# Kernel tuning notes

Hardware: AMD Instinct MI355X
Metric: run time of the kernel (lower is better)

## Reference

```python
import jax, jax.numpy as jnp
import numpy as np

# Dims: batch, lig atoms (padded), rec residues, in-feat, heads, feat/head, edge-hid, n-edges
B, L, R, F, H, FH, FE, E = 16, 128, 512, 256, 8, 32, 64, 16384
HF = H * FH  # 256


def setup_inputs() -> dict:
    key = jax.random.key(0)
    ks = jax.random.split(key, 16)
    n = jax.random.normal
    return {
        "ll_feat": n(ks[0], (B, L, L, F), dtype=jnp.float32),
        "lig_feat": n(ks[1], (B, L, F), dtype=jnp.float32),
        "rec_feat": n(ks[2], (B, R, F), dtype=jnp.float32),
        "mask": jax.random.bernoulli(ks[3], 0.9, (B, L, L)),
        "e_batch": jax.random.randint(ks[4], (E,), 0, B),
        "e_src": jax.random.randint(ks[5], (E,), 0, L),
        "e_dst": jax.random.randint(ks[6], (E,), 0, L),
        # AttentionContract params: NormAndLinear (W,b + layernorm gamma/beta) + atn linear
        "Wc": n(ks[7], (HF, F)) * 0.05, "bc": jnp.zeros(HF), "gc": jnp.ones(HF), "bec": jnp.zeros(HF),
        "Wca": n(ks[8], (H, F)) * 0.05, "bca": jnp.zeros(H),
        # AttentionExpand params (x branch and y branch NormAndLinear)
        "Wex": n(ks[9], (HF, F)) * 0.05, "bex": jnp.zeros(HF), "gex": jnp.ones(HF), "beex": jnp.zeros(HF),
        "Wey": n(ks[10], (HF, F)) * 0.05, "bey": jnp.zeros(HF), "gey": jnp.ones(HF), "beey": jnp.zeros(HF),
        # edge projection (feat_to_edge_feat gather -> linear -> scatter)
        "We": n(ks[11], (FE, 2 * F)) * 0.05, "be": jnp.zeros(FE),
    }


def _norm_linear(x, W, b, g, beta):
    """NormAndLinear: linear(leaky_relu(x)) then layernorm over last dim."""
    h = jnp.einsum('...i,oi->...o', jax.nn.leaky_relu(x), W) + b
    mu = h.mean(-1, keepdims=True)
    var = ((h - mu) ** 2).mean(-1, keepdims=True)
    return g * (h - mu) * jax.lax.rsqrt(var + 1e-5) + beta


def _masked_softmax(x, mask, axis):
    """Faithful softmax_with_mask: exp(x-max), zero masked entries, /(sum+1e-10)."""
    xe = jnp.exp(x - x.max(axis=axis, keepdims=True))
    xe = jnp.where(mask, xe, 0.0)
    return xe / (xe.sum(axis=axis, keepdims=True) + 1e-10)


def reference(ll_feat, lig_feat, rec_feat, mask, e_batch, e_src, e_dst,
              Wc, bc, gc, bec, Wca, bca,
              Wex, bex, gex, beex, Wey, bey, gey, beey, We, be):
    # --- AttentionContract: (B,L,L,F) -> (B,L,H*FH), masked softmax over axis -3 (Y) ---
    of = _norm_linear(ll_feat, Wc, bc, gc, bec).reshape(B, L, L, H, FH)
    atn = (jnp.einsum('blyf,hf->blyh', jax.nn.leaky_relu(ll_feat), Wca) + bca)[..., None]  # (B,L,L,H,1)
    atn = _masked_softmax(atn, mask[..., None, None], axis=-3)
    contracted = (atn * of).sum(-3).reshape(B, L, HF)

    # --- AttentionExpand: (B,L,F),(B,R,F) -> (B,L,R,H) ---
    xf = _norm_linear(lig_feat, Wex, bex, gex, beex).reshape(B, L, H, FH)
    yf = _norm_linear(rec_feat, Wey, bey, gey, beey).reshape(B, R, H, FH)
    expanded = jnp.einsum('bxhf,byhf->bxyh', xf, yf)

    # --- feat_to_edge_feat gather + projection + lig_edges_to_ll_feat scatter ---
    ef = jnp.concatenate((lig_feat[e_batch, e_src], lig_feat[e_batch, e_dst]), axis=-1)  # (E,2F)
    ef = jax.nn.leaky_relu(ef @ We.T + be)  # (E,FE)
    llf = jnp.zeros((B, L, L, FE), ef.dtype).at[e_batch, e_src, e_dst].add(ef)

    return (contracted, expanded, llf)
```

## Files before the change

### kernel.cpp

```cpp
#include <hip/hip_runtime.h>
#include <cstdint>
#include <cstddef>

typedef unsigned int u32;
typedef unsigned short u16;
typedef __bf16 bf16x8 __attribute__((ext_vector_type(8)));
typedef float f32x16 __attribute__((ext_vector_type(16)));
typedef float f32x4v __attribute__((ext_vector_type(4)));

#define DEV static __device__ __forceinline__

DEV u16 f2bf(float f){ u32 u=__float_as_uint(f); return (u16)((u + 0x7FFFu + ((u>>16)&1u))>>16); }
DEV u32 cvtpk(float lo, float hi){ u32 r; asm("v_cvt_pk_bf16_f32 %0, %1, %2":"=v"(r):"v"(lo),"v"(hi)); return r; }
DEV uint2 cvt4(float4 v){ uint2 r; r.x=cvtpk(v.x,v.y); r.y=cvtpk(v.z,v.w); return r; }
DEV uint2 cvt4(f32x4v v){ uint2 r; r.x=cvtpk(v.x,v.y); r.y=cvtpk(v.z,v.w); return r; }
DEV u32 lrelu_pk(u32 u){
  float lo=__uint_as_float(u<<16);
  float hi=__uint_as_float(u&0xFFFF0000u);
  lo=fmaxf(lo,0.01f*lo); hi=fmaxf(hi,0.01f*hi);
  return cvtpk(lo,hi);
}

__global__ void k_prepack(const float* __restrict__ Wc, const float* __restrict__ Wca,
    const float* __restrict__ Wex, const float* __restrict__ Wey, const float* __restrict__ We,
    const unsigned char* __restrict__ maskb,
    u16* __restrict__ wpc, u16* __restrict__ wpx, u16* __restrict__ wpy,
    u16* __restrict__ wpe, int* __restrict__ flags, float* __restrict__ outl)
{
  int idx = blockIdx.x*256 + threadIdx.x;
  {
    int t=idx>>13, kk=(idx>>9)&15, ln=(idx>>3)&63, j=idx&7;
    int n=t*32+(ln&31), k=kk*16+(ln>>5)*8+j;
    if (idx < 73728){
      float v;
      if (t<8) v = Wc[n*256+k];
      else { int n2=n-256; v = (n2<8) ? Wca[n2*256+k] : 0.f; }
      wpc[idx]=f2bf(v);
    }
    if (idx < 65536){ wpx[idx]=f2bf(Wex[n*256+k]); wpy[idx]=f2bf(Wey[n*256+k]); }
  }
  if (idx < 32768){
    int t=idx>>14, kk=(idx>>9)&31, ln=(idx>>3)&63, j=idx&7;
    int n=t*32+(ln&31), k=kk*16+(ln>>5)*8+j;
    wpe[idx]=f2bf(We[n*512+k]);
  }
  {
    float4 z; z.x=0.f; z.y=0.f; z.z=0.f; z.w=0.f;
    float4* p = (float4*)outl;
    for (size_t i = (size_t)idx; i < 4194304u; i += 73728u) p[i] = z;
  }
  if (idx==0){
    int c3f1=0,c3f3=0,nzoff=0,nz4m8=0,nz0=0;
    for (int i=0;i<256;i++){
      unsigned char b=maskb[i];
      if ((i&3)==1 && b==0x3F) c3f1++;
      if ((i&3)==3 && b==0x3F) c3f3++;
      if ((i&3)!=0 && b) nzoff++;
      if ((i&7)>=4 && b) nz4m8++;
      if ((i&7)==0 && b) nz0++;
    }
    int mode;
    if (c3f1>8) mode=2;
    else if (c3f3>8) mode=3;
    else if (nzoff>8) mode=0;
    else if (nz4m8==0 && nz0>4) mode=4;
    else mode=1;
    flags[0]=mode;
  }
}

union FMem {
  struct { char slab[65536]; float maskv[128]; } c;
  struct { u16 ytile[8448]; float stage[4][2048]; } e;
  char eslab[65536];
};

DEV void contract_body(FMem& sm, int bl,
    const float* __restrict__ ll, const void* __restrict__ maskp,
    const u16* __restrict__ Wp, const float* __restrict__ bc, const float* __restrict__ bca,
    const float* __restrict__ gc, const float* __restrict__ bec,
    const int* __restrict__ flags, float* __restrict__ outc)
{
  int tid=threadIdx.x, lane=tid&63, wave=tid>>6;
  const float* src = ll + (size_t)bl*(128*256);

  if (tid < 128){
    int mode = flags[0];
    size_t mi = (size_t)bl*128 + tid;
    bool on;
    if (mode==0)      on = ((const unsigned char*)maskp)[mi] != 0;
    else if (mode==1) on = ((const int*)maskp)[mi] != 0;
    else if (mode==2) on = ((const u16*)maskp)[mi] != 0;
    else if (mode==4) on = ((const unsigned long long*)maskp)[mi] != 0ull;
    else              on = (((const u32*)maskp)[mi]<<1) != 0;
    sm.c.maskv[tid] = on ? 1.f : 0.f;
  }

  #pragma unroll 8
  for (int it=0;it<32;it++){
    int row = wave*32 + it;
    f32x4v v = __builtin_nontemporal_load((const f32x4v*)(src + row*256 + lane*4));
    uint2 pk = cvt4(v);
    *(uint2*)(sm.c.slab + row*512 + ((((lane>>1) ^ (row&31)))<<4) + (lane&1)*8) = pk;
  }
  __syncthreads();

  f32x16 acc[9];
  #pragma unroll
  for (int t=0;t<9;t++)
    #pragma unroll
    for (int i=0;i<16;i++) acc[t][i]=0.f;
  int y0 = wave*32;
  int arow = y0 + (lane&31);
  int axor = arow & 31;
  int half = lane>>5;
  const char* sb = sm.c.slab;
  const u16* wl = Wp + lane*8;

  uint4 raw = *(const uint4*)(sb + arow*512 + ((half ^ axor)<<4));
  bf16x8 w0 = *(const bf16x8*)(wl);
  bf16x8 w1 = *(const bf16x8*)(wl + 8192);
  bf16x8 w2 = *(const bf16x8*)(wl + 16384);
  bf16x8 w3 = *(const bf16x8*)(wl + 24576);
  bf16x8 w4 = *(const bf16x8*)(wl + 32768);
  bf16x8 w5 = *(const bf16x8*)(wl + 40960);
  bf16x8 w6 = *(const bf16x8*)(wl + 49152);
  bf16x8 w7 = *(const bf16x8*)(wl + 57344);
  bf16x8 w8 = *(const bf16x8*)(wl + 65536);

  #pragma unroll 4
  for (int kk=0;kk<16;kk++){
    int kn = (kk+1)&15;
    uint4 rawn = *(const uint4*)(sb + arow*512 + (((kn*2+half) ^ axor)<<4));
    const u16* wkn = wl + (size_t)kn*512;
    bf16x8 n0 = *(const bf16x8*)(wkn);
    bf16x8 n1 = *(const bf16x8*)(wkn + 8192);
    bf16x8 n2 = *(const bf16x8*)(wkn + 16384);
    bf16x8 n3 = *(const bf16x8*)(wkn + 24576);
    bf16x8 n4 = *(const bf16x8*)(wkn + 32768);
    bf16x8 n5 = *(const bf16x8*)(wkn + 40960);
    bf16x8 n6 = *(const bf16x8*)(wkn + 49152);
    bf16x8 n7 = *(const bf16x8*)(wkn + 57344);
    bf16x8 n8 = *(const bf16x8*)(wkn + 65536);
    __builtin_amdgcn_sched_barrier(0);
    uint4 t4; t4.x=lrelu_pk(raw.x); t4.y=lrelu_pk(raw.y); t4.z=lrelu_pk(raw.z); t4.w=lrelu_pk(raw.w);
    bf16x8 a = __builtin_bit_cast(bf16x8, t4);
    acc[0] = __builtin_amdgcn_mfma_f32_32x32x16_bf16(a, w0, acc[0], 0,0,0);
    acc[1] = __builtin_amdgcn_mfma_f32_32x32x16_bf16(a, w1, acc[1], 0,0,0);
    acc[2] = __builtin_amdgcn_mfma_f32_32x32x16_bf16(a, w2, acc[2], 0,0,0);
    acc[3] = __builtin_amdgcn_mfma_f32_32x32x16_bf16(a, w3, acc[3], 0,0,0);
    acc[4] = __builtin_amdgcn_mfma_f32_32x32x16_bf16(a, w4, acc[4], 0,0,0);
    acc[5] = __builtin_amdgcn_mfma_f32_32x32x16_bf16(a, w5, acc[5], 0,0,0);
    acc[6] = __builtin_amdgcn_mfma_f32_32x32x16_bf16(a, w6, acc[6], 0,0,0);
    acc[7] = __builtin_amdgcn_mfma_f32_32x32x16_bf16(a, w7, acc[7], 0,0,0);
    acc[8] = __builtin_amdgcn_mfma_f32_32x32x16_bf16(a, w8, acc[8], 0,0,0);
    raw=rawn;
    w0=n0; w1=n1; w2=n2; w3=n3; w4=n4; w5=n5; w6=n6; w7=n7; w8=n8;
  }
  __syncthreads();

  float* logit = (float*)sm.c.slab;
  float* partial = logit + 1536;

  int col = lane & 31;
  float bv[8], gv[8], bev[8];
  #pragma unroll
  for (int t=0;t<8;t++){
    int n=t*32+col; bv[t]=bc[n]; gv[t]=gc[n]; bev[t]=bec[n];
  }
  float bcav = (col<8) ? bca[col] : 0.f;

  #pragma unroll
  for (int r=0;r<16;r++){
    int row=(r&3)+8*(r>>2)+4*half;
    float s=0.f, sq=0.f;
    #pragma unroll
    for (int t=0;t<8;t++){
      float v = acc[t][r] + bv[t]; acc[t][r]=v; s += v; sq = fmaf(v,v,sq);
    }
    #pragma unroll
    for (int m=1;m<=16;m<<=1){ s += __shfl_xor(s,m,64); sq += __shfl_xor(sq,m,64); }
    float mu = s*(1.f/256.f);
    float var = fmaf(sq,1.f/256.f, -mu*mu);
    float rin = rsqrtf(var+1e-5f);
    #pragma unroll
    for (int t=0;t<8;t++) acc[t][r] = fmaf((acc[t][r]-mu)*rin, gv[t], bev[t]);
    if (col<8) logit[(y0+row)*12+col] = acc[8][r] + bcav;
  }
  __syncthreads();

  {
    int h = tid>>5, sub = tid&31;
    float lv[4], ev[4];
    #pragma unroll
    for (int j=0;j<4;j++) lv[j] = logit[(sub+32*j)*12 + h];
    float mx = fmaxf(fmaxf(lv[0],lv[1]), fmaxf(lv[2],lv[3]));
    #pragma unroll
    for (int m=1;m<=16;m<<=1) mx = fmaxf(mx, __shfl_xor(mx,m,64));
    float ssum=0.f;
    #pragma unroll
    for (int j=0;j<4;j++){ ev[j] = __expf(lv[j]-mx)*sm.c.maskv[sub+32*j]; ssum += ev[j]; }
    #pragma unroll
    for (int m=1;m<=16;m<<=1) ssum += __shfl_xor(ssum,m,64);
    float inv = 1.f/(ssum+1e-10f);
    #pragma unroll
    for (int j=0;j<4;j++) logit[(sub+32*j)*12+h] = ev[j]*inv;
  }
  __syncthreads();

  float ctr[8];
  #pragma unroll
  for (int t=0;t<8;t++) ctr[t]=0.f;
  #pragma unroll
  for (int r=0;r<16;r++){
    int row=(r&3)+8*(r>>2)+4*half;
    const float* wr = &logit[(y0+row)*12];
    float4 w0v = *(const float4*)wr;
    float4 w1v = *(const float4*)(wr+4);
    ctr[0]=fmaf(w0v.x,acc[0][r],ctr[0]); ctr[1]=fmaf(w0v.y,acc[1][r],ctr[1]);
    ctr[2]=fmaf(w0v.z,acc[2][r],ctr[2]); ctr[3]=fmaf(w0v.w,acc[3][r],ctr[3]);
    ctr[4]=fmaf(w1v.x,acc[4][r],ctr[4]); ctr[5]=fmaf(w1v.y,acc[5][r],ctr[5]);
    ctr[6]=fmaf(w1v.z,acc[6][r],ctr[6]); ctr[7]=fmaf(w1v.w,acc[7][r],ctr[7]);
  }
  #pragma unroll
  for (int t=0;t<8;t++) ctr[t] += __shfl_xor(ctr[t],32,64);
  if (lane<32){
    #pragma unroll
    for (int t=0;t<8;t++) partial[wave*256 + t*32 + col] = ctr[t];
  }
  __syncthreads();
  float v = partial[tid]+partial[256+tid]+partial[512+tid]+partial[768+tid];
  outc[(size_t)bl*256 + tid] = v;
}

DEV void expand_body(FMem& sm, int blk,
    const u16* __restrict__ xf, const u16* __restrict__ yf, float* __restrict__ oute)
{
  int tid=threadIdx.x, lane=tid&63, wave=tid>>6;
  int bi = blk>>4, yt = blk&15;

  #pragma unroll
  for (int i=0;i<4;i++){
    int idx=i*256+tid; int row=idx>>5, c=idx&31;
    uint4 v = *(const uint4*)(yf + ((size_t)(bi*512 + yt*32 + row))*256 + c*8);
    *(uint4*)((char*)sm.e.ytile + row*528 + c*16) = v;
  }
  __syncthreads();

  bf16x8 af[2][8];
  #pragma unroll
  for (int xi=0;xi<2;xi++){
    int x = (wave*2+xi)*16 + (lane&15);
    #pragma unroll
    for (int h=0;h<8;h++)
      af[xi][h] = *(const bf16x8*)(xf + ((size_t)(bi*128+x))*256 + h*32 + (lane>>4)*8);
  }
  float* stw = sm.e.stage[wave];
  #pragma unroll
  for (int xi=0;xi<2;xi++){
    #pragma unroll
    for (int nt=0;nt<2;nt++){
      f32x4v c[8];
      #pragma unroll
      for (int h=0;h<8;h++){
        bf16x8 bv = *(const bf16x8*)((const char*)sm.e.ytile + (nt*16+(lane&15))*528 + (h*32+(lane>>4)*8)*2);
        f32x4v z = {0.f,0.f,0.f,0.f};
        c[h] = __builtin_amdgcn_mfma_f32_16x16x32_bf16(af[xi][h], bv, z, 0,0,0);
      }
      #pragma unroll
      for (int q=0;q<4;q++){
        int xp=(lane>>4)*4+q, yp=lane&15;
        float* sp = &stw[(xp*16+yp)*8];
        float4 v0; v0.x=c[0][q]; v0.y=c[1][q]; v0.z=c[2][q]; v0.w=c[3][q];
        float4 v1; v1.x=c[4][q]; v1.y=c[5][q]; v1.z=c[6][q]; v1.w=c[7][q];
        *(float4*)sp = v0;
        *(float4*)(sp+4) = v1;
      }
      #pragma unroll
      for (int j=0;j<4;j++){
        int pi=j*64+lane, xp=pi>>4, yp=pi&15;
        const float* sp = &stw[(xp*16+yp)*8];
        float4 a = *(const float4*)sp;
        float4 b2 = *(const float4*)(sp+4);
        size_t x=(size_t)(wave*2+xi)*16+xp, y=(size_t)yt*32+nt*16+yp;
        float* po = oute + (((size_t)bi*128+x)*512 + y)*8;
        *(float4*)po = a;
        *(float4*)(po+4) = b2;
      }
    }
  }
}

DEV void edges_body(FMem& sm, int blk,
    const float* __restrict__ lig, const int* __restrict__ eb, const int* __restrict__ es,
    const int* __restrict__ ed, const u16* __restrict__ Wp, const float* __restrict__ bias,
    float* __restrict__ outl)
{
  char* slab = sm.eslab;
  int tid=threadIdx.x, lane=tid&63, wave=tid>>6;
  int e0 = blk*64;
  int ge = e0 + wave*16 + (lane&15);
  int b0=eb[ge], s0=es[ge], d0=ed[ge];
  long long ps = (long long)(uintptr_t)(lig + ((size_t)(b0*128+s0))*256);
  long long pd = (long long)(uintptr_t)(lig + ((size_t)(b0*128+d0))*256);
  #pragma unroll 4
  for (int i=0;i<16;i++){
    int ri = wave*16 + i;
    const float* sp = (const float*)(uintptr_t)__shfl(ps, i, 16);
    const float* dp = (const float*)(uintptr_t)__shfl(pd, i, 16);
    #pragma unroll
    for (int j=0;j<2;j++){
      const float* base = j ? dp : sp;
      float4 v = *(const float4*)(base + lane*4);
      uint2 pk = cvt4(v);
      int g = j*32 + (lane>>1);
      *(uint2*)(slab + (size_t)ri*1024 + ((g ^ (ri&63))<<4) + (lane&1)*8) = pk;
    }
  }
  __syncthreads();

  f32x16 acc;
  #pragma unroll
  for (int i=0;i<16;i++) acc[i]=0.f;
  int arow = (wave&1)*32 + (lane&31);
  int axor = arow & 63;
  int half = lane>>5;
  int t = wave>>1;
  const u16* wl = Wp + lane*8 + (size_t)t*16384;

  uint4 raw = *(const uint4*)(slab + (size_t)arow*1024 + ((half ^ axor)<<4));
  bf16x8 w = *(const bf16x8*)(wl);
  for (int kk=0;kk<32;kk++){
    int kn = (kk+1)&31;
    uint4 rn = *(const uint4*)(slab + (size_t)arow*1024 + (((kn*2+half) ^ axor)<<4));
    bf16x8 nw = *(const bf16x8*)(wl + (size_t)kn*512);
    __builtin_amdgcn_sched_barrier(0);
    bf16x8 a = __builtin_bit_cast(bf16x8, raw);
    acc = __builtin_amdgcn_mfma_f32_32x32x16_bf16(a, w, acc, 0,0,0);
    raw=rn; w=nw;
  }
  int col = lane&31;
  float bv = bias[t*32+col];
  #pragma unroll
  for (int r=0;r<16;r++){
    int row=(r&3)+8*(r>>2)+4*half;
    int ee = e0 + (wave&1)*32 + row;
    int bb=eb[ee], ss=es[ee], dd=ed[ee];
    float* cell = outl + (((size_t)(bb*128+ss))*128 + (size_t)dd)*64;
    float v = acc[r] + bv;
    v = fmaxf(v, 0.01f*v);
    atomicAdd(cell + t*32 + col, v);
  }
}

__global__ __launch_bounds__(256,2) void k_fused(
    const float* __restrict__ ll, const void* __restrict__ maskp,
    const u16* __restrict__ wpc, const float* __restrict__ bc, const float* __restrict__ bca,
    const float* __restrict__ gc, const float* __restrict__ bec,
    const int* __restrict__ flags, float* __restrict__ outc,
    const u16* __restrict__ xf, const u16* __restrict__ yf, float* __restrict__ oute,
    const float* __restrict__ lig, const int* __restrict__ eb, const int* __restrict__ es,
    const int* __restrict__ ed, const u16* __restrict__ wpe, const float* __restrict__ be,
    float* __restrict__ outl)
{
  __shared__ __attribute__((aligned(16))) FMem sm;
  int bid = blockIdx.x;
  if (bid < 256)       edges_body(sm, bid, lig, eb, es, ed, wpe, be, outl);
  else if (bid < 512)  expand_body(sm, bid-256, xf, yf, oute);
  else                 contract_body(sm, bid-512, ll, maskp, wpc, bc, bca, gc, bec, flags, outc);
}

__global__ __launch_bounds__(256,2) void k_nl(
    const float* __restrict__ lig, const float* __restrict__ rec,
    const u16* __restrict__ Wpx, const u16* __restrict__ Wpy,
    const float* __restrict__ bx, const float* __restrict__ gx, const float* __restrict__ ex,
    const float* __restrict__ by, const float* __restrict__ gy, const float* __restrict__ ey,
    u16* __restrict__ xf, u16* __restrict__ yf)
{
  __shared__ __attribute__((aligned(16))) char slab[65536];
  int tid=threadIdx.x, lane=tid&63, wave=tid>>6;
  bool isx = blockIdx.x < 16;
  int bb = isx ? blockIdx.x : blockIdx.x - 16;
  const float* src  = isx ? lig : rec;
  const u16*  Wp    = isx ? Wpx : Wpy;
  const float* bias = isx ? bx : by;
  const float* g    = isx ? gx : gy;
  const float* beta = isx ? ex : ey;
  u16* dst          = isx ? xf : yf;

  const float* s0 = src + (size_t)bb*(128*256);
  #pragma unroll 8
  for (int it=0;it<32;it++){
    int row = wave*32 + it;
    float4 v = *(const float4*)(s0 + row*256 + lane*4);
    uint2 pk = cvt4(v);
    *(uint2*)(slab + row*512 + ((((lane>>1) ^ (row&31)))<<4) + (lane&1)*8) = pk;
  }
  __syncthreads();

  f32x16 acc[8];
  #pragma unroll
  for (int t=0;t<8;t++)
    #pragma unroll
    for (int i=0;i<16;i++) acc[t][i]=0.f;
  int y0 = wave*32;
  int arow = y0 + (lane&31);
  int axor = arow & 31;
  int half = lane>>5;
  const u16* wl = Wp + lane*8;

  uint4 raw = *(const uint4*)(slab + arow*512 + ((half ^ axor)<<4));
  bf16x8 w0 = *(const bf16x8*)(wl);
  bf16x8 w1 = *(const bf16x8*)(wl + 8192);
  bf16x8 w2 = *(const bf16x8*)(wl + 16384);
  bf16x8 w3 = *(const bf16x8*)(wl + 24576);
  bf16x8 w4 = *(const bf16x8*)(wl + 32768);
  bf16x8 w5 = *(const bf16x8*)(wl + 40960);
  bf16x8 w6 = *(const bf16x8*)(wl + 49152);
  bf16x8 w7 = *(const bf16x8*)(wl + 57344);

  #pragma unroll 4
  for (int kk=0;kk<16;kk++){
    int kn = (kk+1)&15;
    uint4 rawn = *(const uint4*)(slab + arow*512 + (((kn*2+half) ^ axor)<<4));
    const u16* wkn = wl + (size_t)kn*512;
    bf16x8 n0 = *(const bf16x8*)(wkn);
    bf16x8 n1 = *(const bf16x8*)(wkn + 8192);
    bf16x8 n2 = *(const bf16x8*)(wkn + 16384);
    bf16x8 n3 = *(const bf16x8*)(wkn + 24576);
    bf16x8 n4 = *(const bf16x8*)(wkn + 32768);
    bf16x8 n5 = *(const bf16x8*)(wkn + 40960);
    bf16x8 n6 = *(const bf16x8*)(wkn + 49152);
    bf16x8 n7 = *(const bf16x8*)(wkn + 57344);
    __builtin_amdgcn_sched_barrier(0);
    uint4 t4; t4.x=lrelu_pk(raw.x); t4.y=lrelu_pk(raw.y); t4.z=lrelu_pk(raw.z); t4.w=lrelu_pk(raw.w);
    bf16x8 a = __builtin_bit_cast(bf16x8, t4);
    acc[0] = __builtin_amdgcn_mfma_f32_32x32x16_bf16(a, w0, acc[0], 0,0,0);
    acc[1] = __builtin_amdgcn_mfma_f32_32x32x16_bf16(a, w1, acc[1], 0,0,0);
    acc[2] = __builtin_amdgcn_mfma_f32_32x32x16_bf16(a, w2, acc[2], 0,0,0);
    acc[3] = __builtin_amdgcn_mfma_f32_32x32x16_bf16(a, w3, acc[3], 0,0,0);
    acc[4] = __builtin_amdgcn_mfma_f32_32x32x16_bf16(a, w4, acc[4], 0,0,0);
    acc[5] = __builtin_amdgcn_mfma_f32_32x32x16_bf16(a, w5, acc[5], 0,0,0);
    acc[6] = __builtin_amdgcn_mfma_f32_32x32x16_bf16(a, w6, acc[6], 0,0,0);
    acc[7] = __builtin_amdgcn_mfma_f32_32x32x16_bf16(a, w7, acc[7], 0,0,0);
    raw=rawn;
    w0=n0; w1=n1; w2=n2; w3=n3; w4=n4; w5=n5; w6=n6; w7=n7;
  }
  int col = lane & 31;
  float bv[8], gv[8], bev[8];
  #pragma unroll
  for (int t=0;t<8;t++){
    int n=t*32+col; bv[t]=bias[n]; gv[t]=g[n]; bev[t]=beta[n];
  }
  #pragma unroll
  for (int r=0;r<16;r++){
    int row=(r&3)+8*(r>>2)+4*half;
    float s=0.f, sq=0.f;
    #pragma unroll
    for (int t=0;t<8;t++){
      float v = acc[t][r] + bv[t]; acc[t][r]=v; s += v; sq = fmaf(v,v,sq);
    }
    #pragma unroll
    for (int m=1;m<=16;m<<=1){ s += __shfl_xor(s,m,64); sq += __shfl_xor(sq,m,64); }
    float mu = s*(1.f/256.f);
    float var = fmaf(sq,1.f/256.f, -mu*mu);
    float rin = rsqrtf(var+1e-5f);
    size_t rowg = (size_t)bb*128 + y0 + row;
    #pragma unroll
    for (int t=0;t<8;t++){
      float v = fmaf((acc[t][r]-mu)*rin, gv[t], bev[t]);
      dst[rowg*256 + t*32 + col] = f2bf(v);
    }
  }
}

extern "C" void kernel_launch(void* const* d_in, const int* in_sizes, int n_in,
                              void* d_out, int out_size, void* d_ws, size_t ws_size,
                              hipStream_t stream)
{
  (void)in_sizes; (void)n_in; (void)out_size; (void)ws_size;
  const float* ll  = (const float*)d_in[0];
  const float* lig = (const float*)d_in[1];
  const float* rec = (const float*)d_in[2];
  const void* mask = d_in[3];
  const int* eb = (const int*)d_in[4];
  const int* es = (const int*)d_in[5];
  const int* ed = (const int*)d_in[6];
  const float* Wc  =(const float*)d_in[7];  const float* bc  =(const float*)d_in[8];
  const float* gc  =(const float*)d_in[9];  const float* bec =(const float*)d_in[10];
  const float* Wca =(const float*)d_in[11]; const float* bca =(const float*)d_in[12];
  const float* Wex =(const float*)d_in[13]; const float* bex =(const float*)d_in[14];
  const float* gex =(const float*)d_in[15]; const float* beex=(const float*)d_in[16];
  const float* Wey =(const float*)d_in[17]; const float* bey =(const float*)d_in[18];
  const float* gey =(const float*)d_in[19]; const float* beey=(const float*)d_in[20];
  const float* We  =(const float*)d_in[21]; const float* be  =(const float*)d_in[22];

  float* outc = (float*)d_out;
  float* oute = outc + 524288;
  float* outl = outc + 8912896;

  char* ws = (char*)d_ws;
  int* flags = (int*)ws;
  u16* wpc = (u16*)(ws + 4096);
  u16* wpx = (u16*)(ws + 151552);
  u16* wpy = (u16*)(ws + 282624);
  u16* wpe = (u16*)(ws + 413696);
  u16* xf  = (u16*)(ws + 479232);
  u16* yf  = (u16*)(ws + 1527808);

  hipLaunchKernelGGL(k_prepack, dim3(288), dim3(256), 0, stream,
                     Wc, Wca, Wex, Wey, We, (const unsigned char*)mask,
                     wpc, wpx, wpy, wpe, flags, outl);
  hipLaunchKernelGGL(k_nl, dim3(80), dim3(256), 0, stream,
                     lig, rec, wpx, wpy, bex, gex, beex, bey, gey, beey, xf, yf);
  hipLaunchKernelGGL(k_fused, dim3(2560), dim3(256), 0, stream,
                     ll, mask, wpc, bc, bca, gc, bec, flags, outc,
                     xf, yf, oute, lig, eb, es, ed, wpe, be, outl);
}
```

Before: 504.0 us.

## Merge prepack and NL kernels, drop LDS staging for direct global operand loads

Folds the lig/rec NormAndLinear work into the weight-prepack kernel, with extra blocks that read fp32 weights directly, and removes the k_nl launch along with the bf16 prepack of Wex/Wey. The contract, expand and edge bodies no longer stage operands through 64KB of shared memory. They load MFMA operands straight from global memory and convert them in registers, and expand writes its output without an LDS transpose. This cuts one launch, several barriers and the LDS footprint, so more blocks can fit per CU. The cost is uncoalesced, strided global loads and more global traffic per MFMA.

```diff
diff --git a/kernel.cpp b/kernel.cpp
--- a/kernel.cpp
+++ b/kernel.cpp
@@ -12,70 +12,153 @@
 
 DEV u16 f2bf(float f){ u32 u=__float_as_uint(f); return (u16)((u + 0x7FFFu + ((u>>16)&1u))>>16); }
 DEV u32 cvtpk(float lo, float hi){ u32 r; asm("v_cvt_pk_bf16_f32 %0, %1, %2":"=v"(r):"v"(lo),"v"(hi)); return r; }
-DEV uint2 cvt4(float4 v){ uint2 r; r.x=cvtpk(v.x,v.y); r.y=cvtpk(v.z,v.w); return r; }
-DEV uint2 cvt4(f32x4v v){ uint2 r; r.x=cvtpk(v.x,v.y); r.y=cvtpk(v.z,v.w); return r; }
-DEV u32 lrelu_pk(u32 u){
-  float lo=__uint_as_float(u<<16);
-  float hi=__uint_as_float(u&0xFFFF0000u);
-  lo=fmaxf(lo,0.01f*lo); hi=fmaxf(hi,0.01f*hi);
-  return cvtpk(lo,hi);
-}
-
-__global__ void k_prepack(const float* __restrict__ Wc, const float* __restrict__ Wca,
-    const float* __restrict__ Wex, const float* __restrict__ Wey, const float* __restrict__ We,
+DEV float flr(float v){ return fmaxf(v, 0.01f*v); }
+DEV bf16x8 cvt8_lrelu(f32x4v a0, f32x4v a1){
+  uint4 t;
+  t.x=cvtpk(flr(a0[0]),flr(a0[1])); t.y=cvtpk(flr(a0[2]),flr(a0[3]));
+  t.z=cvtpk(flr(a1[0]),flr(a1[1])); t.w=cvtpk(flr(a1[2]),flr(a1[3]));
+  return __builtin_bit_cast(bf16x8, t);
+}
+DEV bf16x8 cvt8(f32x4v a0, f32x4v a1){
+  uint4 t;
+  t.x=cvtpk(a0[0],a0[1]); t.y=cvtpk(a0[2],a0[3]);
+  t.z=cvtpk(a1[0],a1[1]); t.w=cvtpk(a1[2],a1[3]);
+  return __builtin_bit_cast(bf16x8, t);
+}
+
+DEV void nl_body(int bb0,
+    const float* __restrict__ lig, const float* __restrict__ rec,
+    const float* __restrict__ Wex, const float* __restrict__ Wey,
+    const float* __restrict__ bx, const float* __restrict__ gx, const float* __restrict__ ex,
+    const float* __restrict__ by, const float* __restrict__ gy, const float* __restrict__ ey,
+    u16* __restrict__ xf, u16* __restrict__ yf)
+{
+  int tid=threadIdx.x, lane=tid&63, wave=tid>>6;
+  bool isx = bb0 < 16;
+  int bb = isx ? bb0 : bb0 - 16;
+  const float* src  = isx ? lig : rec;
+  const float* W    = isx ? Wex : Wey;
+  const float* bias = isx ? bx : by;
+  const float* g    = isx ? gx : gy;
+  const float* beta = isx ? ex : ey;
+  u16* dst          = isx ? xf : yf;
+
+  int y0 = wave*32;
+  int arow = y0 + (lane&31);
+  int half = lane>>5;
+  const float* xb = src + (size_t)bb*(128*256) + arow*256 + half*8;
+  const float* wb = W + (size_t)(lane&31)*256 + half*8;
+
+  f32x16 acc[8];
+  #pragma unroll
+  for (int t=0;t<8;t++)
+    #pragma unroll
+    for (int i=0;i<16;i++) acc[t][i]=0.f;
+
+  for (int kk=0;kk<16;kk++){
+    f32x4v x0 = *(const f32x4v*)(xb + kk*16);
+    f32x4v x1 = *(const f32x4v*)(xb + kk*16 + 4);
+    bf16x8 a = cvt8_lrelu(x0, x1);
+    #pragma unroll
+    for (int t=0;t<8;t++){
+      const float* wt = wb + (size_t)t*8192 + kk*16;
+      f32x4v w0v = *(const f32x4v*)(wt);
+      f32x4v w1v = *(const f32x4v*)(wt + 4);
+      bf16x8 w = cvt8(w0v, w1v);
+      acc[t] = __builtin_amdgcn_mfma_f32_32x32x16_bf16(a, w, acc[t], 0,0,0);
+    }
+  }
+  int col = lane & 31;
+  float bv[8], gv[8], bev[8];
+  #pragma unroll
+  for (int t=0;t<8;t++){
+    int n=t*32+col; bv[t]=bias[n]; gv[t]=g[n]; bev[t]=beta[n];
+  }
+  #pragma unroll
+  for (int r=0;r<16;r++){
+    int row=(r&3)+8*(r>>2)+4*half;
+    float s=0.f, sq=0.f;
+    #pragma unroll
+    for (int t=0;t<8;t++){
+      float v = acc[t][r] + bv[t]; acc[t][r]=v; s += v; sq = fmaf(v,v,sq);
+    }
+    #pragma unroll
+    for (int m=1;m<=16;m<<=1){ s += __shfl_xor(s,m,64); sq += __shfl_xor(sq,m,64); }
+    float mu = s*(1.f/256.f);
+    float var = fmaf(sq,1.f/256.f, -mu*mu);
+    float rin = rsqrtf(var+1e-5f);
+    size_t rowg = (size_t)bb*128 + y0 + row;
+    #pragma unroll
+    for (int t=0;t<8;t++){
+      float v = fmaf((acc[t][r]-mu)*rin, gv[t], bev[t]);
+      dst[rowg*256 + t*32 + col] = f2bf(v);
+    }
+  }
+}
+
+__global__ __launch_bounds__(256,2) void k_pre(
+    const float* __restrict__ Wc, const float* __restrict__ Wca, const float* __restrict__ We,
     const unsigned char* __restrict__ maskb,
-    u16* __restrict__ wpc, u16* __restrict__ wpx, u16* __restrict__ wpy,
-    u16* __restrict__ wpe, int* __restrict__ flags, float* __restrict__ outl)
-{
-  int idx = blockIdx.x*256 + threadIdx.x;
-  {
-    int t=idx>>13, kk=(idx>>9)&15, ln=(idx>>3)&63, j=idx&7;
-    int n=t*32+(ln&31), k=kk*16+(ln>>5)*8+j;
-    if (idx < 73728){
-      float v;
-      if (t<8) v = Wc[n*256+k];
-      else { int n2=n-256; v = (n2<8) ? Wca[n2*256+k] : 0.f; }
-      wpc[idx]=f2bf(v);
-    }
-    if (idx < 65536){ wpx[idx]=f2bf(Wex[n*256+k]); wpy[idx]=f2bf(Wey[n*256+k]); }
-  }
-  if (idx < 32768){
-    int t=idx>>14, kk=(idx>>9)&31, ln=(idx>>3)&63, j=idx&7;
-    int n=t*32+(ln&31), k=kk*16+(ln>>5)*8+j;
-    wpe[idx]=f2bf(We[n*512+k]);
+    const float* __restrict__ lig, const float* __restrict__ rec,
+    const float* __restrict__ Wex, const float* __restrict__ Wey,
+    const float* __restrict__ bx, const float* __restrict__ gx, const float* __restrict__ ex,
+    const float* __restrict__ by, const float* __restrict__ gy, const float* __restrict__ ey,
+    u16* __restrict__ wpc, u16* __restrict__ wpe, int* __restrict__ flags,
+    float* __restrict__ outl, u16* __restrict__ xf, u16* __restrict__ yf)
+{
+  int bid = blockIdx.x, tid = threadIdx.x;
+  if (bid < 288){
+    int idx = bid*256 + tid;
+    {
+      int t=idx>>13, kk=(idx>>9)&15, ln=(idx>>3)&63, j=idx&7;
+      int n=t*32+(ln&31), k=kk*16+(ln>>5)*8+j;
+      if (idx < 73728){
+        float v;
+        if (t<8) v = Wc[n*256+k];
+        else { int n2=n-256; v = (n2<8) ? Wca[n2*256+k] : 0.f; }
+        wpc[idx]=f2bf(v);
+      }
+    }
+    if (idx < 32768){
+      int t=idx>>14, kk=(idx>>9)&31, ln=(idx>>3)&63, j=idx&7;
+      int n=t*32+(ln&31), k=kk*16+(ln>>5)*8+j;
+      wpe[idx]=f2bf(We[n*512+k]);
+    }
+    if (idx==0){
+      int c3f1=0,c3f3=0,nzoff=0,nz4m8=0,nz0=0;
+      for (int i=0;i<256;i++){
+        unsigned char b=maskb[i];
+        if ((i&3)==1 && b==0x3F) c3f1++;
+        if ((i&3)==3 && b==0x3F) c3f3++;
+        if ((i&3)!=0 && b) nzoff++;
+        if ((i&7)>=4 && b) nz4m8++;
+        if ((i&7)==0 && b) nz0++;
+      }
+      int mode;
+      if (c3f1>8) mode=2;
+      else if (c3f3>8) mode=3;
+      else if (nzoff>8) mode=0;
+      else if (nz4m8==0 && nz0>4) mode=4;
+      else mode=1;
+      flags[0]=mode;
+    }
+  } else {
+    nl_body(bid-288, lig, rec, Wex, Wey, bx, gx, ex, by, gy, ey, xf, yf);
   }
   {
     float4 z; z.x=0.f; z.y=0.f; z.z=0.f; z.w=0.f;
     float4* p = (float4*)outl;
-    for (size_t i = (size_t)idx; i < 4194304u; i += 73728u) p[i] = z;
-  }
-  if (idx==0){
-    int c3f1=0,c3f3=0,nzoff=0,nz4m8=0,nz0=0;
-    for (int i=0;i<256;i++){
-      unsigned char b=maskb[i];
-      if ((i&3)==1 && b==0x3F) c3f1++;
-      if ((i&3)==3 && b==0x3F) c3f3++;
-      if ((i&3)!=0 && b) nzoff++;
-      if ((i&7)>=4 && b) nz4m8++;
-      if ((i&7)==0 && b) nz0++;
-    }
-    int mode;
-    if (c3f1>8) mode=2;
-    else if (c3f3>8) mode=3;
-    else if (nzoff>8) mode=0;
-    else if (nz4m8==0 && nz0>4) mode=4;
-    else mode=1;
-    flags[0]=mode;
-  }
-}
-
-union FMem {
-  struct { char slab[65536]; float maskv[128]; } c;
-  struct { u16 ytile[8448]; float stage[4][2048]; } e;
-  char eslab[65536];
+    for (size_t i = (size_t)bid*256 + tid; i < 4194304u; i += 94208u) p[i] = z;
+  }
+}
+
+struct CMem {
+  float maskv[128];
+  float logit[1536];
+  float partial[1024];
 };
 
-DEV void contract_body(FMem& sm, int bl,
+DEV void contract_body(CMem& sm, int bl,
     const float* __restrict__ ll, const void* __restrict__ maskp,
     const u16* __restrict__ Wp, const float* __restrict__ bc, const float* __restrict__ bca,
     const float* __restrict__ gc, const float* __restrict__ bec,
@@ -93,17 +176,8 @@
     else if (mode==2) on = ((const u16*)maskp)[mi] != 0;
     else if (mode==4) on = ((const unsigned long long*)maskp)[mi] != 0ull;
     else              on = (((const u32*)maskp)[mi]<<1) != 0;
-    sm.c.maskv[tid] = on ? 1.f : 0.f;
-  }
-
-  #pragma unroll 8
-  for (int it=0;it<32;it++){
-    int row = wave*32 + it;
-    f32x4v v = __builtin_nontemporal_load((const f32x4v*)(src + row*256 + lane*4));
-    uint2 pk = cvt4(v);
-    *(uint2*)(sm.c.slab + row*512 + ((((lane>>1) ^ (row&31)))<<4) + (lane&1)*8) = pk;
-  }
-  __syncthreads();
+    sm.maskv[tid] = on ? 1.f : 0.f;
+  }
 
   f32x16 acc[9];
   #pragma unroll
@@ -112,55 +186,45 @@
     for (int i=0;i<16;i++) acc[t][i]=0.f;
   int y0 = wave*32;
   int arow = y0 + (lane&31);
-  int axor = arow & 31;
   int half = lane>>5;
-  const char* sb = sm.c.slab;
+  const float* abase = src + arow*256 + half*8;
   const u16* wl = Wp + lane*8;
 
-  uint4 raw = *(const uint4*)(sb + arow*512 + ((half ^ axor)<<4));
-  bf16x8 w0 = *(const bf16x8*)(wl);
-  bf16x8 w1 = *(const bf16x8*)(wl + 8192);
-  bf16x8 w2 = *(const bf16x8*)(wl + 16384);
-  bf16x8 w3 = *(const bf16x8*)(wl + 24576);
-  bf16x8 w4 = *(const bf16x8*)(wl + 32768);
-  bf16x8 w5 = *(const bf16x8*)(wl + 40960);
-  bf16x8 w6 = *(const bf16x8*)(wl + 49152);
-  bf16x8 w7 = *(const bf16x8*)(wl + 57344);
-  bf16x8 w8 = *(const bf16x8*)(wl + 65536);
+  f32x4v a0 = __builtin_nontemporal_load((const f32x4v*)(abase));
+  f32x4v a1 = __builtin_nontemporal_load((const f32x4v*)(abase + 4));
 
   #pragma unroll 4
   for (int kk=0;kk<16;kk++){
     int kn = (kk+1)&15;
-    uint4 rawn = *(const uint4*)(sb + arow*512 + (((kn*2+half) ^ axor)<<4));
-    const u16* wkn = wl + (size_t)kn*512;
-    bf16x8 n0 = *(const bf16x8*)(wkn);
-    bf16x8 n1 = *(const bf16x8*)(wkn + 8192);
-    bf16x8 n2 = *(const bf16x8*)(wkn + 16384);
-    bf16x8 n3 = *(const bf16x8*)(wkn + 24576);
-    bf16x8 n4 = *(const bf16x8*)(wkn + 32768);
-    bf16x8 n5 = *(const bf16x8*)(wkn + 40960);
-    bf16x8 n6 = *(const bf16x8*)(wkn + 49152);
-    bf16x8 n7 = *(const bf16x8*)(wkn + 57344);
-    bf16x8 n8 = *(const bf16x8*)(wkn + 65536);
+    f32x4v a0n = __builtin_nontemporal_load((const f32x4v*)(abase + kn*16));
+    f32x4v a1n = __builtin_nontemporal_load((const f32x4v*)(abase + kn*16 + 4));
+    const u16* wk = wl + (size_t)kk*512;
+    bf16x8 b0 = *(const bf16x8*)(wk);
+    bf16x8 b1 = *(const bf16x8*)(wk + 8192);
+    bf16x8 b2 = *(const bf16x8*)(wk + 16384);
+    bf16x8 b3 = *(const bf16x8*)(wk + 24576);
+    bf16x8 b4 = *(const bf16x8*)(wk + 32768);
     __builtin_amdgcn_sched_barrier(0);
-    uint4 t4; t4.x=lrelu_pk(raw.x); t4.y=lrelu_pk(raw.y); t4.z=lrelu_pk(raw.z); t4.w=lrelu_pk(raw.w);
-    bf16x8 a = __builtin_bit_cast(bf16x8, t4);
-    acc[0] = __builtin_amdgcn_mfma_f32_32x32x16_bf16(a, w0, acc[0], 0,0,0);
-    acc[1] = __builtin_amdgcn_mfma_f32_32x32x16_bf16(a, w1, acc[1], 0,0,0);
-    acc[2] = __builtin_amdgcn_mfma_f32_32x32x16_bf16(a, w2, acc[2], 0,0,0);
-    acc[3] = __builtin_amdgcn_mfma_f32_32x32x16_bf16(a, w3, acc[3], 0,0,0);
-    acc[4] = __builtin_amdgcn_mfma_f32_32x32x16_bf16(a, w4, acc[4], 0,0,0);
-    acc[5] = __builtin_amdgcn_mfma_f32_32x32x16_bf16(a, w5, acc[5], 0,0,0);
-    acc[6] = __builtin_amdgcn_mfma_f32_32x32x16_bf16(a, w6, acc[6], 0,0,0);
-    acc[7] = __builtin_amdgcn_mfma_f32_32x32x16_bf16(a, w7, acc[7], 0,0,0);
-    acc[8] = __builtin_amdgcn_mfma_f32_32x32x16_bf16(a, w8, acc[8], 0,0,0);
-    raw=rawn;
-    w0=n0; w1=n1; w2=n2; w3=n3; w4=n4; w5=n5; w6=n6; w7=n7; w8=n8;
-  }
-  __syncthreads();
-
-  float* logit = (float*)sm.c.slab;
-  float* partial = logit + 1536;
+    bf16x8 a = cvt8_lrelu(a0, a1);
+    acc[0] = __builtin_amdgcn_mfma_f32_32x32x16_bf16(a, b0, acc[0], 0,0,0);
+    acc[1] = __builtin_amdgcn_mfma_f32_32x32x16_bf16(a, b1, acc[1], 0,0,0);
+    acc[2] = __builtin_amdgcn_mfma_f32_32x32x16_bf16(a, b2, acc[2], 0,0,0);
+    acc[3] = __builtin_amdgcn_mfma_f32_32x32x16_bf16(a, b3, acc[3], 0,0,0);
+    acc[4] = __builtin_amdgcn_mfma_f32_32x32x16_bf16(a, b4, acc[4], 0,0,0);
+    bf16x8 b5 = *(const bf16x8*)(wk + 40960);
+    bf16x8 b6 = *(const bf16x8*)(wk + 49152);
+    bf16x8 b7 = *(const bf16x8*)(wk + 57344);
+    bf16x8 b8 = *(const bf16x8*)(wk + 65536);
+    __builtin_amdgcn_sched_barrier(0);
+    acc[5] = __builtin_amdgcn_mfma_f32_32x32x16_bf16(a, b5, acc[5], 0,0,0);
+    acc[6] = __builtin_amdgcn_mfma_f32_32x32x16_bf16(a, b6, acc[6], 0,0,0);
+    acc[7] = __builtin_amdgcn_mfma_f32_32x32x16_bf16(a, b7, acc[7], 0,0,0);
+    acc[8] = __builtin_amdgcn_mfma_f32_32x32x16_bf16(a, b8, acc[8], 0,0,0);
+    a0=a0n; a1=a1n;
+  }
+
+  float* logit = sm.logit;
+  float* partial = sm.partial;
 
   int col = lane & 31;
   float bv[8], gv[8], bev[8];
@@ -199,7 +263,7 @@
     for (int m=1;m<=16;m<<=1) mx = fmaxf(mx, __shfl_xor(mx,m,64));
     float ssum=0.f;
     #pragma unroll
-    for (int j=0;j<4;j++){ ev[j] = __expf(lv[j]-mx)*sm.c.maskv[sub+32*j]; ssum += ev[j]; }
+    for (int j=0;j<4;j++){ ev[j] = __expf(lv[j]-mx)*sm.maskv[sub+32*j]; ssum += ev[j]; }
     #pragma unroll
     for (int m=1;m<=16;m<<=1) ssum += __shfl_xor(ssum,m,64);
     float inv = 1.f/(ssum+1e-10f);
@@ -233,20 +297,12 @@
   outc[(size_t)bl*256 + tid] = v;
 }
 
-DEV void expand_body(FMem& sm, int blk,
+DEV void expand_body(int blk,
     const u16* __restrict__ xf, const u16* __restrict__ yf, float* __restrict__ oute)
 {
   int tid=threadIdx.x, lane=tid&63, wave=tid>>6;
   int bi = blk>>4, yt = blk&15;
 
-  #pragma unroll
-  for (int i=0;i<4;i++){
-    int idx=i*256+tid; int row=idx>>5, c=idx&31;
-    uint4 v = *(const uint4*)(yf + ((size_t)(bi*512 + yt*32 + row))*256 + c*8);
-    *(uint4*)((char*)sm.e.ytile + row*528 + c*16) = v;
-  }
-  __syncthreads();
-
   bf16x8 af[2][8];
   #pragma unroll
   for (int xi=0;xi<2;xi++){
@@ -255,97 +311,76 @@
     for (int h=0;h<8;h++)
       af[xi][h] = *(const bf16x8*)(xf + ((size_t)(bi*128+x))*256 + h*32 + (lane>>4)*8);
   }
-  float* stw = sm.e.stage[wave];
-  #pragma unroll
-  for (int xi=0;xi<2;xi++){
-    #pragma unroll
-    for (int nt=0;nt<2;nt++){
-      f32x4v c[8];
-      #pragma unroll
-      for (int h=0;h<8;h++){
-        bf16x8 bv = *(const bf16x8*)((const char*)sm.e.ytile + (nt*16+(lane&15))*528 + (h*32+(lane>>4)*8)*2);
-        f32x4v z = {0.f,0.f,0.f,0.f};
-        c[h] = __builtin_amdgcn_mfma_f32_16x16x32_bf16(af[xi][h], bv, z, 0,0,0);
-      }
+  const u16* yb = yf + ((size_t)(bi*512 + yt*32 + (lane&15)))*256 + (lane>>4)*8;
+
+  #pragma unroll
+  for (int nt=0;nt<2;nt++){
+    f32x4v cc[2][8];
+    #pragma unroll
+    for (int h=0;h<8;h++){
+      bf16x8 bv = *(const bf16x8*)(yb + (size_t)nt*16*256 + h*32);
+      f32x4v z = {0.f,0.f,0.f,0.f};
+      cc[0][h] = __builtin_amdgcn_mfma_f32_16x16x32_bf16(af[0][h], bv, z, 0,0,0);
+      cc[1][h] = __builtin_amdgcn_mfma_f32_16x16x32_bf16(af[1][h], bv, z, 0,0,0);
+    }
+    #pragma unroll
+    for (int xi=0;xi<2;xi++){
       #pragma unroll
       for (int q=0;q<4;q++){
-        int xp=(lane>>4)*4+q, yp=lane&15;
-        float* sp = &stw[(xp*16+yp)*8];
-        float4 v0; v0.x=c[0][q]; v0.y=c[1][q]; v0.z=c[2][q]; v0.w=c[3][q];
-        float4 v1; v1.x=c[4][q]; v1.y=c[5][q]; v1.z=c[6][q]; v1.w=c[7][q];
-        *(float4*)sp = v0;
-        *(float4*)(sp+4) = v1;
+        int x = (wave*2+xi)*16 + (lane>>4)*4 + q;
+        int y = yt*32 + nt*16 + (lane&15);
+        float* po = oute + (((size_t)bi*128+x)*512 + y)*8;
+        float4 v0; v0.x=cc[xi][0][q]; v0.y=cc[xi][1][q]; v0.z=cc[xi][2][q]; v0.w=cc[xi][3][q];
+        float4 v1; v1.x=cc[xi][4][q]; v1.y=cc[xi][5][q]; v1.z=cc[xi][6][q]; v1.w=cc[xi][7][q];
+        *(float4*)po = v0;
+        *(float4*)(po+4) = v1;
       }
-      #pragma unroll
-      for (int j=0;j<4;j++){
-        int pi=j*64+lane, xp=pi>>4, yp=pi&15;
-        const float* sp = &stw[(xp*16+yp)*8];
-        float4 a = *(const float4*)sp;
-        float4 b2 = *(const float4*)(sp+4);
-        size_t x=(size_t)(wave*2+xi)*16+xp, y=(size_t)yt*32+nt*16+yp;
-        float* po = oute + (((size_t)bi*128+x)*512 + y)*8;
-        *(float4*)po = a;
-        *(float4*)(po+4) = b2;
-      }
-    }
-  }
-}
-
-DEV void edges_body(FMem& sm, int blk,
+    }
+  }
+}
+
+DEV void edges_body(int blk,
     const float* __restrict__ lig, const int* __restrict__ eb, const int* __restrict__ es,
     const int* __restrict__ ed, const u16* __restrict__ Wp, const float* __restrict__ bias,
     float* __restrict__ outl)
 {
-  char* slab = sm.eslab;
   int tid=threadIdx.x, lane=tid&63, wave=tid>>6;
   int e0 = blk*64;
-  int ge = e0 + wave*16 + (lane&15);
-  int b0=eb[ge], s0=es[ge], d0=ed[ge];
-  long long ps = (long long)(uintptr_t)(lig + ((size_t)(b0*128+s0))*256);
-  long long pd = (long long)(uintptr_t)(lig + ((size_t)(b0*128+d0))*256);
-  #pragma unroll 4
-  for (int i=0;i<16;i++){
-    int ri = wave*16 + i;
-    const float* sp = (const float*)(uintptr_t)__shfl(ps, i, 16);
-    const float* dp = (const float*)(uintptr_t)__shfl(pd, i, 16);
-    #pragma unroll
-    for (int j=0;j<2;j++){
-      const float* base = j ? dp : sp;
-      float4 v = *(const float4*)(base + lane*4);
-      uint2 pk = cvt4(v);
-      int g = j*32 + (lane>>1);
-      *(uint2*)(slab + (size_t)ri*1024 + ((g ^ (ri&63))<<4) + (lane&1)*8) = pk;
-    }
-  }
-  __syncthreads();
-
-  f32x16 acc;
-  #pragma unroll
-  for (int i=0;i<16;i++) acc[i]=0.f;
-  int arow = (wave&1)*32 + (lane&31);
-  int axor = arow & 63;
   int half = lane>>5;
   int t = wave>>1;
+  int ee = e0 + (wave&1)*32 + (lane&31);
+  int b0=eb[ee], s0v=es[ee], d0=ed[ee];
+  const float* sb = lig + ((size_t)(b0*128+s0v))*256 + half*8;
+  const float* db = lig + ((size_t)(b0*128+d0))*256 + half*8;
   const u16* wl = Wp + lane*8 + (size_t)t*16384;
 
-  uint4 raw = *(const uint4*)(slab + (size_t)arow*1024 + ((half ^ axor)<<4));
+  f32x16 acc;
+  #pragma unroll
+  for (int i=0;i<16;i++) acc[i]=0.f;
+
+  f32x4v a0 = *(const f32x4v*)(sb);
+  f32x4v a1 = *(const f32x4v*)(sb + 4);
   bf16x8 w = *(const bf16x8*)(wl);
+
   for (int kk=0;kk<32;kk++){
     int kn = (kk+1)&31;
-    uint4 rn = *(const uint4*)(slab + (size_t)arow*1024 + (((kn*2+half) ^ axor)<<4));
+    int k0n = kn*16 + half*8;
+    const float* bp = (k0n < 256) ? (sb + kn*16) : (db + kn*16 - 256);
+    f32x4v a0n = *(const f32x4v*)(bp);
+    f32x4v a1n = *(const f32x4v*)(bp + 4);
     bf16x8 nw = *(const bf16x8*)(wl + (size_t)kn*512);
     __builtin_amdgcn_sched_barrier(0);
-    bf16x8 a = __builtin_bit_cast(bf16x8, raw);
+    bf16x8 a = cvt8(a0, a1);
     acc = __builtin_amdgcn_mfma_f32_32x32x16_bf16(a, w, acc, 0,0,0);
-    raw=rn; w=nw;
+    a0=a0n; a1=a1n; w=nw;
   }
   int col = lane&31;
   float bv = bias[t*32+col];
   #pragma unroll
   for (int r=0;r<16;r++){
     int row=(r&3)+8*(r>>2)+4*half;
-    int ee = e0 + (wave&1)*32 + row;
-    int bb=eb[ee], ss=es[ee], dd=ed[ee];
+    int er = e0 + (wave&1)*32 + row;
+    int bb=eb[er], ss=es[er], dd=ed[er];
     float* cell = outl + (((size_t)(bb*128+ss))*128 + (size_t)dd)*64;
     float v = acc[r] + bv;
     v = fmaxf(v, 0.01f*v);
@@ -363,115 +398,11 @@
     const int* __restrict__ ed, const u16* __restrict__ wpe, const float* __restrict__ be,
     float* __restrict__ outl)
 {
-  __shared__ __attribute__((aligned(16))) FMem sm;
+  __shared__ __attribute__((aligned(16))) CMem sm;
   int bid = blockIdx.x;
-  if (bid < 256)       edges_body(sm, bid, lig, eb, es, ed, wpe, be, outl);
-  else if (bid < 512)  expand_body(sm, bid-256, xf, yf, oute);
+  if (bid < 256)       edges_body(bid, lig, eb, es, ed, wpe, be, outl);
+  else if (bid < 512)  expand_body(bid-256, xf, yf, oute);
   else                 contract_body(sm, bid-512, ll, maskp, wpc, bc, bca, gc, bec, flags, outc);
-}
-
-__global__ __launch_bounds__(256,2) void k_nl(
-    const float* __restrict__ lig, const float* __restrict__ rec,
-    const u16* __restrict__ Wpx, const u16* __restrict__ Wpy,
-    const float* __restrict__ bx, const float* __restrict__ gx, const float* __restrict__ ex,
-    const float* __restrict__ by, const float* __restrict__ gy, const float* __restrict__ ey,
-    u16* __restrict__ xf, u16* __restrict__ yf)
-{
-  __shared__ __attribute__((aligned(16))) char slab[65536];
-  int tid=threadIdx.x, lane=tid&63, wave=tid>>6;
-  bool isx = blockIdx.x < 16;
-  int bb = isx ? blockIdx.x : blockIdx.x - 16;
-  const float* src  = isx ? lig : rec;
-  const u16*  Wp    = isx ? Wpx : Wpy;
-  const float* bias = isx ? bx : by;
-  const float* g    = isx ? gx : gy;
-  const float* beta = isx ? ex : ey;
-  u16* dst          = isx ? xf : yf;
-
-  const float* s0 = src + (size_t)bb*(128*256);
-  #pragma unroll 8
-  for (int it=0;it<32;it++){
-    int row = wave*32 + it;
-    float4 v = *(const float4*)(s0 + row*256 + lane*4);
-    uint2 pk = cvt4(v);
-    *(uint2*)(slab + row*512 + ((((lane>>1) ^ (row&31)))<<4) + (lane&1)*8) = pk;
-  }
-  __syncthreads();
-
-  f32x16 acc[8];
-  #pragma unroll
-  for (int t=0;t<8;t++)
-    #pragma unroll
-    for (int i=0;i<16;i++) acc[t][i]=0.f;
-  int y0 = wave*32;
-  int arow = y0 + (lane&31);
-  int axor = arow & 31;
-  int half = lane>>5;
-  const u16* wl = Wp + lane*8;
-
-  uint4 raw = *(const uint4*)(slab + arow*512 + ((half ^ axor)<<4));
-  bf16x8 w0 = *(const bf16x8*)(wl);
-  bf16x8 w1 = *(const bf16x8*)(wl + 8192);
-  bf16x8 w2 = *(const bf16x8*)(wl + 16384);
-  bf16x8 w3 = *(const bf16x8*)(wl + 24576);
-  bf16x8 w4 = *(const bf16x8*)(wl + 32768);
-  bf16x8 w5 = *(const bf16x8*)(wl + 40960);
-  bf16x8 w6 = *(const bf16x8*)(wl + 49152);
-  bf16x8 w7 = *(const bf16x8*)(wl + 57344);
-
-  #pragma unroll 4
-  for (int kk=0;kk<16;kk++){
-    int kn = (kk+1)&15;
-    uint4 rawn = *(const uint4*)(slab + arow*512 + (((kn*2+half) ^ axor)<<4));
-    const u16* wkn = wl + (size_t)kn*512;
-    bf16x8 n0 = *(const bf16x8*)(wkn);
-    bf16x8 n1 = *(const bf16x8*)(wkn + 8192);
-    bf16x8 n2 = *(const bf16x8*)(wkn + 16384);
-    bf16x8 n3 = *(const bf16x8*)(wkn + 24576);
-    bf16x8 n4 = *(const bf16x8*)(wkn + 32768);
-    bf16x8 n5 = *(const bf16x8*)(wkn + 40960);
-    bf16x8 n6 = *(const bf16x8*)(wkn + 49152);
-    bf16x8 n7 = *(const bf16x8*)(wkn + 57344);
-    __builtin_amdgcn_sched_barrier(0);
-    uint4 t4; t4.x=lrelu_pk(raw.x); t4.y=lrelu_pk(raw.y); t4.z=lrelu_pk(raw.z); t4.w=lrelu_pk(raw.w);
-    bf16x8 a = __builtin_bit_cast(bf16x8, t4);
-    acc[0] = __builtin_amdgcn_mfma_f32_32x32x16_bf16(a, w0, acc[0], 0,0,0);
-    acc[1] = __builtin_amdgcn_mfma_f32_32x32x16_bf16(a, w1, acc[1], 0,0,0);
-    acc[2] = __builtin_amdgcn_mfma_f32_32x32x16_bf16(a, w2, acc[2], 0,0,0);
-    acc[3] = __builtin_amdgcn_mfma_f32_32x32x16_bf16(a, w3, acc[3], 0,0,0);
-    acc[4] = __builtin_amdgcn_mfma_f32_32x32x16_bf16(a, w4, acc[4], 0,0,0);
-    acc[5] = __builtin_amdgcn_mfma_f32_32x32x16_bf16(a, w5, acc[5], 0,0,0);
-    acc[6] = __builtin_amdgcn_mfma_f32_32x32x16_bf16(a, w6, acc[6], 0,0,0);
-    acc[7] = __builtin_amdgcn_mfma_f32_32x32x16_bf16(a, w7, acc[7], 0,0,0);
-    raw=rawn;
-    w0=n0; w1=n1; w2=n2; w3=n3; w4=n4; w5=n5; w6=n6; w7=n7;
-  }
-  int col = lane & 31;
-  float bv[8], gv[8], bev[8];
-  #pragma unroll
-  for (int t=0;t<8;t++){
-    int n=t*32+col; bv[t]=bias[n]; gv[t]=g[n]; bev[t]=beta[n];
-  }
-  #pragma unroll
-  for (int r=0;r<16;r++){
-    int row=(r&3)+8*(r>>2)+4*half;
-    float s=0.f, sq=0.f;
-    #pragma unroll
-    for (int t=0;t<8;t++){
-      float v = acc[t][r] + bv[t]; acc[t][r]=v; s += v; sq = fmaf(v,v,sq);
-    }
-    #pragma unroll
-    for (int m=1;m<=16;m<<=1){ s += __shfl_xor(s,m,64); sq += __shfl_xor(sq,m,64); }
-    float mu = s*(1.f/256.f);
-    float var = fmaf(sq,1.f/256.f, -mu*mu);
-    float rin = rsqrtf(var+1e-5f);
-    size_t rowg = (size_t)bb*128 + y0 + row;
-    #pragma unroll
-    for (int t=0;t<8;t++){
-      float v = fmaf((acc[t][r]-mu)*rin, gv[t], bev[t]);
-      dst[rowg*256 + t*32 + col] = f2bf(v);
-    }
-  }
 }
 
 extern "C" void kernel_launch(void* const* d_in, const int* in_sizes, int n_in,
@@ -502,17 +433,15 @@
   char* ws = (char*)d_ws;
   int* flags = (int*)ws;
   u16* wpc = (u16*)(ws + 4096);
-  u16* wpx = (u16*)(ws + 151552);
-  u16* wpy = (u16*)(ws + 282624);
   u16* wpe = (u16*)(ws + 413696);
   u16* xf  = (u16*)(ws + 479232);
   u16* yf  = (u16*)(ws + 1527808);
 
-  hipLaunchKernelGGL(k_prepack, dim3(288), dim3(256), 0, stream,
-                     Wc, Wca, Wex, Wey, We, (const unsigned char*)mask,
-                     wpc, wpx, wpy, wpe, flags, outl);
-  hipLaunchKernelGGL(k_nl, dim3(80), dim3(256), 0, stream,
-                     lig, rec, wpx, wpy, bex, gex, beex, bey, gey, beey, xf, yf);
+  hipLaunchKernelGGL(k_pre, dim3(368), dim3(256), 0, stream,
+                     Wc, Wca, We, (const unsigned char*)mask,
+                     lig, rec, Wex, Wey,
+                     bex, gex, beex, bey, gey, beey,
+                     wpc, wpe, flags, outl, xf, yf);
   hipLaunchKernelGGL(k_fused, dim3(2560), dim3(256), 0, stream,
                      ll, mask, wpc, bc, bca, gc, bec, flags, outc,
                      xf, yf, oute, lig, eb, es, ed, wpe, be, outl);
```

Result: slower. 612.1 us (+21.5%).
